# Performance work log

Hardware: AMD Instinct MI355X
Metric: run time of the kernel (lower is better)

Reference implementation:

```python
import jax, jax.numpy as jnp
import numpy as np

N = 50000
E = 1600000
EP = 500000
D_IN, D_EMB = 64, 32


def setup_inputs() -> dict:
    key = jax.random.key(0)
    ks = jax.random.split(key, 12)
    return {
        "x": jax.random.normal(ks[0], (N, D_IN), dtype=jnp.float32),
        "W1": jax.random.normal(ks[1], (D_IN, D_EMB), dtype=jnp.float32) * (1.0 / np.sqrt(D_IN)),
        "b1": jnp.zeros((D_EMB,), dtype=jnp.float32),
        "W2": jax.random.normal(ks[2], (D_EMB, 2 * D_EMB), dtype=jnp.float32) * (1.0 / np.sqrt(D_EMB)),
        "b2": jnp.zeros((2 * D_EMB,), dtype=jnp.float32),
        "eps": jax.random.normal(ks[3], (N, D_EMB), dtype=jnp.float32),
        "edge_src": jax.random.randint(ks[4], (E,), 0, N, dtype=jnp.int32),
        "edge_dst": jax.random.randint(ks[5], (E,), 0, N, dtype=jnp.int32),
        "pos_src": jax.random.randint(ks[6], (EP,), 0, N, dtype=jnp.int32),
        "pos_dst": jax.random.randint(ks[7], (EP,), 0, N, dtype=jnp.int32),
        "neg_src": jax.random.randint(ks[8], (EP,), 0, N, dtype=jnp.int32),
        "neg_dst": jax.random.randint(ks[9], (EP,), 0, N, dtype=jnp.int32),
    }


def _degree_norms(src, dst, n):
    ones = jnp.ones(src.shape, dtype=jnp.float32)
    out_deg = jax.ops.segment_sum(ones, src, num_segments=n)
    in_deg = jax.ops.segment_sum(ones, dst, num_segments=n)
    # DGL GraphConv norm='both': clamp degrees to >=1, pow(-0.5)
    return jnp.clip(out_deg, 1.0) ** -0.5, jnp.clip(in_deg, 1.0) ** -0.5


def _graph_conv(h, src, dst, norm_src, norm_dst, W, b, n):
    # rst = D_dst^{-1/2} A D_src^{-1/2} h W + b
    msg = (h * norm_src[:, None])[src]                       # [E, d] gather
    agg = jax.ops.segment_sum(msg, dst, num_segments=n)      # [N, d] scatter-add
    return (agg * norm_dst[:, None]) @ W + b


def _dot_predict(z, u, v):
    # u_dot_v: per-edge inner product of endpoint embeddings
    return jnp.sum(z[u] * z[v], axis=-1)


def reference(x, W1, b1, W2, b2, eps, edge_src, edge_dst,
              pos_src, pos_dst, neg_src, neg_dst):
    n = x.shape[0]
    ns, nd = _degree_norms(edge_src, edge_dst, n)
    h = _graph_conv(x, edge_src, edge_dst, ns, nd, W1, b1, n)
    h = jax.nn.relu(h)  # dropout = identity (eval mode)
    h = _graph_conv(h, edge_src, edge_dst, ns, nd, W2, b2, n)
    mu, log_var = jnp.split(h, 2, axis=-1)
    sigma = jnp.exp(log_var / 2.0)
    z = mu + sigma * eps
    pos = _dot_predict(z, pos_src, pos_dst)
    neg = _dot_predict(z, neg_src, neg_dst)
    return pos, neg, mu, sigma
```

## Files before the change

kernel.cpp:

```cpp
#include <hip/hip_runtime.h>
#include <math.h>

#define NN  50000
#define NE  1600000
#define NEP 500000
#define DIN 64
#define DE  32

#define BKT_SH 7
#define NB     391
#define S1B    250
#define CHK    6400
#define HB     128
#define HCHK   12500
#define HWRD   12500
#define XWB    3125

typedef float f4 __attribute__((ext_vector_type(4)));

__device__ __forceinline__ unsigned f2b(float f) {
    unsigned u = __float_as_uint(f);
    return (u + 0x7FFFu + ((u >> 16) & 1u)) >> 16;
}
__device__ __forceinline__ unsigned pack2(float a, float b) {
    return f2b(a) | (f2b(b) << 16);
}
__device__ __forceinline__ float blo(unsigned u) { return __uint_as_float(u << 16); }
__device__ __forceinline__ float bhi(unsigned u) { return __uint_as_float(u & 0xFFFF0000u); }

__global__ __launch_bounds__(256) void k_h1s1(const int* __restrict__ src,
                                              const int* __restrict__ dst,
                                              unsigned* __restrict__ partial,
                                              int* __restrict__ T) {
    __shared__ unsigned h[HWRD];
    int t = threadIdx.x;
    if (blockIdx.x < HB) {
        for (int i = t; i < HWRD; i += 256) h[i] = 0;
        __syncthreads();
        int beg = blockIdx.x * HCHK;
        const int ev = beg + HCHK;
        int i = beg + t;
        for (; i + 1792 < ev; i += 2048) {
            int s0 = src[i],        s1 = src[i + 256],  s2 = src[i + 512],  s3 = src[i + 768];
            int s4 = src[i + 1024], s5 = src[i + 1280], s6 = src[i + 1536], s7 = src[i + 1792];
            atomicAdd(&h[s0 >> 2], 1u << ((s0 & 3) * 8));
            atomicAdd(&h[s1 >> 2], 1u << ((s1 & 3) * 8));
            atomicAdd(&h[s2 >> 2], 1u << ((s2 & 3) * 8));
            atomicAdd(&h[s3 >> 2], 1u << ((s3 & 3) * 8));
            atomicAdd(&h[s4 >> 2], 1u << ((s4 & 3) * 8));
            atomicAdd(&h[s5 >> 2], 1u << ((s5 & 3) * 8));
            atomicAdd(&h[s6 >> 2], 1u << ((s6 & 3) * 8));
            atomicAdd(&h[s7 >> 2], 1u << ((s7 & 3) * 8));
        }
        for (; i < ev; i += 256) {
            int s = src[i];
            atomicAdd(&h[s >> 2], 1u << ((s & 3) * 8));
        }
        __syncthreads();
        unsigned* p = partial + (size_t)blockIdx.x * HWRD;
        for (int i2 = t; i2 < HWRD; i2 += 256) p[i2] = h[i2];
    } else {
        int b = blockIdx.x - HB;
        int* cd = (int*)h;
        for (int i = t; i < NB; i += 256) cd[i] = 0;
        __syncthreads();
        int beg = b * CHK;
        const int ev = beg + CHK;
        int i = beg + t;
        for (; i + 1792 < ev; i += 2048) {
            int d0 = dst[i],        d1 = dst[i + 256],  d2 = dst[i + 512],  d3 = dst[i + 768];
            int d4 = dst[i + 1024], d5 = dst[i + 1280], d6 = dst[i + 1536], d7 = dst[i + 1792];
            atomicAdd(&cd[d0 >> BKT_SH], 1);
            atomicAdd(&cd[d1 >> BKT_SH], 1);
            atomicAdd(&cd[d2 >> BKT_SH], 1);
            atomicAdd(&cd[d3 >> BKT_SH], 1);
            atomicAdd(&cd[d4 >> BKT_SH], 1);
            atomicAdd(&cd[d5 >> BKT_SH], 1);
            atomicAdd(&cd[d6 >> BKT_SH], 1);
            atomicAdd(&cd[d7 >> BKT_SH], 1);
        }
        for (; i < ev; i += 256)
            atomicAdd(&cd[dst[i] >> BKT_SH], 1);
        __syncthreads();
        for (int i2 = t; i2 < NB; i2 += 256) T[b * NB + i2] = cd[i2];
    }
}

__global__ __launch_bounds__(512) void k_s2h(const int* __restrict__ T,
                                             int* __restrict__ Base,
                                             int* __restrict__ BS,
                                             const unsigned* __restrict__ partial,
                                             int* __restrict__ degs) {
    int t = threadIdx.x;
    if (blockIdx.x == 0) {
        __shared__ int tot[512];
        int run = 0;
        if (t < NB) {
            for (int b = 0; b < S1B; b++) {
                Base[b * NB + t] = run;
                run += T[b * NB + t];
            }
        }
        tot[t] = (t < NB) ? run : 0;
        __syncthreads();
        for (int off = 1; off < 512; off <<= 1) {
            int v = (t >= off) ? tot[t - off] : 0;
            __syncthreads();
            tot[t] += v;
            __syncthreads();
        }
        if (t < NB) BS[t] = (t == 0) ? 0 : tot[t - 1];
        if (t == 0) BS[NB] = NE;
    } else {
        int w = (blockIdx.x - 1) * 512 + t;
        if (w < HWRD) {
            int c0 = 0, c1 = 0, c2 = 0, c3 = 0;
#pragma unroll 8
            for (int b = 0; b < HB; b++) {
                unsigned v = partial[(size_t)b * HWRD + w];
                c0 += (int)(v & 0xFFu);
                c1 += (int)((v >> 8) & 0xFFu);
                c2 += (int)((v >> 16) & 0xFFu);
                c3 += (int)(v >> 24);
            }
            ((int4*)degs)[w] = make_int4(c0, c1, c2, c3);
        }
    }
}

__global__ __launch_bounds__(512) void k_s3(const int* __restrict__ src,
                                            const int* __restrict__ dst,
                                            const int* __restrict__ T,
                                            const int* __restrict__ Base,
                                            const int* __restrict__ BS,
                                            unsigned* __restrict__ tmp) {
    __shared__ int scn[512];
    __shared__ int delta[NB];
    __shared__ int cur[NB];
    __shared__ unsigned buf[CHK];
    int t = threadIdx.x;
    int beg = blockIdx.x * CHK;
    scn[t] = (t < NB) ? T[blockIdx.x * NB + t] : 0;
    __syncthreads();
    for (int off = 1; off < 512; off <<= 1) {
        int v = (t >= off) ? scn[t - off] : 0;
        __syncthreads();
        scn[t] += v;
        __syncthreads();
    }
    if (t < NB) {
        int ls = (t == 0) ? 0 : scn[t - 1];
        cur[t] = ls;
        delta[t] = Base[blockIdx.x * NB + t] + BS[t] - ls;
    }
    __syncthreads();
    {
        const int ev = beg + CHK;
        int i = beg + t;
        for (; i + 1536 < ev; i += 2048) {
            int d0 = dst[i],        s0 = src[i];
            int d1 = dst[i + 512],  s1 = src[i + 512];
            int d2 = dst[i + 1024], s2 = src[i + 1024];
            int d3 = dst[i + 1536], s3 = src[i + 1536];
            int l0 = atomicAdd(&cur[d0 >> BKT_SH], 1); buf[l0] = (unsigned)s0 | ((unsigned)d0 << 16);
            int l1 = atomicAdd(&cur[d1 >> BKT_SH], 1); buf[l1] = (unsigned)s1 | ((unsigned)d1 << 16);
            int l2 = atomicAdd(&cur[d2 >> BKT_SH], 1); buf[l2] = (unsigned)s2 | ((unsigned)d2 << 16);
            int l3 = atomicAdd(&cur[d3 >> BKT_SH], 1); buf[l3] = (unsigned)s3 | ((unsigned)d3 << 16);
        }
        for (; i < ev; i += 512) {
            int d = dst[i];
            int s = src[i];
            int lp = atomicAdd(&cur[d >> BKT_SH], 1);
            buf[lp] = (unsigned)s | ((unsigned)d << 16);
        }
    }
    __syncthreads();
    for (int i = t; i < CHK; i += 512) {
        unsigned e = buf[i];
        tmp[delta[e >> (16 + BKT_SH)] + i] = e;
    }
}

__global__ __launch_bounds__(256) void k_s4x(const unsigned* __restrict__ tmp,
                                             const int* __restrict__ BS,
                                             int* __restrict__ csr,
                                             int* __restrict__ rowptr,
                                             const float* __restrict__ x,
                                             const float* __restrict__ W1,
                                             const int* __restrict__ degs,
                                             unsigned* __restrict__ xw1b) {
    __shared__ float sW[DIN * DE];
    int t = threadIdx.x;
    if (blockIdx.x < NB) {
        int* cnt = (int*)sW;
        int* scn = cnt + 128;
        int* cur = cnt + 256;
        int p = blockIdx.x;
        int ebeg = BS[p], eend = BS[p + 1];
        int ne = eend - ebeg;
        if (t < 128) cnt[t] = 0;
        __syncthreads();
        {
            int i = t;
            for (; i + 768 < ne; i += 1024) {
                unsigned e0 = tmp[ebeg + i];
                unsigned e1 = tmp[ebeg + i + 256];
                unsigned e2 = tmp[ebeg + i + 512];
                unsigned e3 = tmp[ebeg + i + 768];
                atomicAdd(&cnt[(e0 >> 16) & 127], 1);
                atomicAdd(&cnt[(e1 >> 16) & 127], 1);
                atomicAdd(&cnt[(e2 >> 16) & 127], 1);
                atomicAdd(&cnt[(e3 >> 16) & 127], 1);
            }
            for (; i < ne; i += 256)
                atomicAdd(&cnt[(tmp[ebeg + i] >> 16) & 127], 1);
        }
        __syncthreads();
        if (t < 128) scn[t] = cnt[t];
        __syncthreads();
        for (int off = 1; off < 128; off <<= 1) {
            int v = 0;
            if (t < 128 && t >= off) v = scn[t - off];
            __syncthreads();
            if (t < 128) scn[t] += v;
            __syncthreads();
        }
        if (t < 128) {
            int ex = (t == 0) ? 0 : scn[t - 1];
            cur[t] = ex;
            int node = (p << BKT_SH) + t;
            if (node < NN) rowptr[node] = ebeg + ex;
        }
        if (p == NB - 1 && t == 0) rowptr[NN] = NE;
        __syncthreads();
        {
            int i = t;
            for (; i + 768 < ne; i += 1024) {
                unsigned e0 = tmp[ebeg + i];
                unsigned e1 = tmp[ebeg + i + 256];
                unsigned e2 = tmp[ebeg + i + 512];
                unsigned e3 = tmp[ebeg + i + 768];
                int l0 = atomicAdd(&cur[(e0 >> 16) & 127], 1); csr[ebeg + l0] = (int)(e0 & 0xFFFFu);
                int l1 = atomicAdd(&cur[(e1 >> 16) & 127], 1); csr[ebeg + l1] = (int)(e1 & 0xFFFFu);
                int l2 = atomicAdd(&cur[(e2 >> 16) & 127], 1); csr[ebeg + l2] = (int)(e2 & 0xFFFFu);
                int l3 = atomicAdd(&cur[(e3 >> 16) & 127], 1); csr[ebeg + l3] = (int)(e3 & 0xFFFFu);
            }
            for (; i < ne; i += 256) {
                unsigned e = tmp[ebeg + i];
                int lp = atomicAdd(&cur[(e >> 16) & 127], 1);
                csr[ebeg + lp] = (int)(e & 0xFFFFu);
            }
        }
    } else {
        for (int i = t; i < DIN * DE; i += 256) sW[i] = W1[i];
        __syncthreads();
        int r  = (blockIdx.x - NB) * 16 + (t >> 4);
        int tc = t & 15;
        const float* xr = x + (size_t)r * DIN;
        float a0 = 0.f, a1 = 0.f;
#pragma unroll
        for (int k = 0; k < DIN; k++) {
            float v = xr[k];
            a0 += v * sW[k * DE + 2 * tc];
            a1 += v * sW[k * DE + 2 * tc + 1];
        }
        float ns = rsqrtf(fmaxf((float)degs[r], 1.0f));
        xw1b[r * 16 + tc] = pack2(a0 * ns, a1 * ns);
    }
}

__device__ __forceinline__ void acc8(float* a, uint4 w) {
    a[0] += blo(w.x); a[1] += bhi(w.x);
    a[2] += blo(w.y); a[3] += bhi(w.y);
    a[4] += blo(w.z); a[5] += bhi(w.z);
    a[6] += blo(w.w); a[7] += bhi(w.w);
}

__device__ __forceinline__ void gather_row(const int* __restrict__ csr,
                                           const uint4* __restrict__ msg,
                                           int beg, int end, int l, float* a) {
    int idx = beg;
    for (; idx + 8 <= end; idx += 8) {
        int s0 = csr[idx],     s1 = csr[idx + 1], s2 = csr[idx + 2], s3 = csr[idx + 3];
        int s4 = csr[idx + 4], s5 = csr[idx + 5], s6 = csr[idx + 6], s7 = csr[idx + 7];
        uint4 w0 = msg[s0 * 4 + l];
        uint4 w1 = msg[s1 * 4 + l];
        uint4 w2 = msg[s2 * 4 + l];
        uint4 w3 = msg[s3 * 4 + l];
        uint4 w4 = msg[s4 * 4 + l];
        uint4 w5 = msg[s5 * 4 + l];
        uint4 w6 = msg[s6 * 4 + l];
        uint4 w7 = msg[s7 * 4 + l];
        acc8(a, w0); acc8(a, w1); acc8(a, w2); acc8(a, w3);
        acc8(a, w4); acc8(a, w5); acc8(a, w6); acc8(a, w7);
    }
    for (; idx + 4 <= end; idx += 4) {
        int s0 = csr[idx], s1 = csr[idx + 1], s2 = csr[idx + 2], s3 = csr[idx + 3];
        uint4 w0 = msg[s0 * 4 + l];
        uint4 w1 = msg[s1 * 4 + l];
        uint4 w2 = msg[s2 * 4 + l];
        uint4 w3 = msg[s3 * 4 + l];
        acc8(a, w0); acc8(a, w1); acc8(a, w2); acc8(a, w3);
    }
    for (; idx < end; idx++) {
        uint4 w = msg[csr[idx] * 4 + l];
        acc8(a, w);
    }
}

__global__ __launch_bounds__(256) void k_g1(const int* __restrict__ rowptr,
                                            const int* __restrict__ csr,
                                            const uint4* __restrict__ msg,
                                            const int* __restrict__ degs,
                                            const float* __restrict__ b1,
                                            uint4* __restrict__ out) {
    int t = blockIdx.x * 256 + threadIdx.x;
    int r = t >> 3;
    int l = t & 3;
    int h = (t >> 2) & 1;
    if (r >= NN) return;
    int beg = rowptr[r];
    int end = rowptr[r + 1];
    int mid = beg + ((end - beg) >> 1);
    float a[8] = {0, 0, 0, 0, 0, 0, 0, 0};
    gather_row(csr, msg, h ? mid : beg, h ? end : mid, l, a);
#pragma unroll
    for (int k = 0; k < 8; k++) a[k] += __shfl_xor(a[k], 4);
    if (h) return;
    float scd = rsqrtf(fmaxf((float)(end - beg), 1.0f));
    float scs = rsqrtf(fmaxf((float)degs[r], 1.0f));
    const float4* b14 = (const float4*)b1;
    float4 bb0 = b14[2 * l], bb1 = b14[2 * l + 1];
    float o0 = fmaxf(scd * a[0] + bb0.x, 0.f) * scs;
    float o1 = fmaxf(scd * a[1] + bb0.y, 0.f) * scs;
    float o2 = fmaxf(scd * a[2] + bb0.z, 0.f) * scs;
    float o3 = fmaxf(scd * a[3] + bb0.w, 0.f) * scs;
    float o4 = fmaxf(scd * a[4] + bb1.x, 0.f) * scs;
    float o5 = fmaxf(scd * a[5] + bb1.y, 0.f) * scs;
    float o6 = fmaxf(scd * a[6] + bb1.z, 0.f) * scs;
    float o7 = fmaxf(scd * a[7] + bb1.w, 0.f) * scs;
    out[r * 4 + l] = make_uint4(pack2(o0, o1), pack2(o2, o3), pack2(o4, o5), pack2(o6, o7));
}

__global__ __launch_bounds__(256) void k_g2f(const int* __restrict__ rowptr,
                                             const int* __restrict__ csr,
                                             const uint4* __restrict__ msg,
                                             const float* __restrict__ W2,
                                             const float* __restrict__ b2,
                                             const float* __restrict__ eps,
                                             float* __restrict__ mu,
                                             float* __restrict__ sigma,
                                             unsigned* __restrict__ zb) {
    __shared__ float sW[DE * 64];
    __shared__ float sb[64];
    int t = threadIdx.x;
    for (int i = t; i < DE * 64; i += 256) sW[i] = W2[i];
    if (t < 64) sb[t] = b2[t];
    __syncthreads();
    int g = blockIdx.x * 256 + t;
    int r = g >> 3;
    int l = g & 3;
    int j = g & 7;
    int h = (g >> 2) & 1;
    if (r >= NN) return;
    int beg = rowptr[r];
    int end = rowptr[r + 1];
    int mid = beg + ((end - beg) >> 1);
    float a[8] = {0, 0, 0, 0, 0, 0, 0, 0};
    gather_row(csr, msg, h ? mid : beg, h ? end : mid, l, a);
#pragma unroll
    for (int k = 0; k < 8; k++) a[k] += __shfl_xor(a[k], 4);
    float scd = rsqrtf(fmaxf((float)(end - beg), 1.0f));
#pragma unroll
    for (int k = 0; k < 8; k++) a[k] *= scd;
    int cbase = 8 * j;
    float o3[8];
#pragma unroll
    for (int c = 0; c < 8; c++) o3[c] = sb[cbase + c];
#pragma unroll
    for (int d = 0; d < 4; d++) {
        int kb = 8 * (l ^ d);
#pragma unroll
        for (int k = 0; k < 8; k++) {
            float av = (d == 0) ? a[k] : __shfl_xor(a[k], d);
            const float* wrow = sW + (kb + k) * 64 + cbase;
#pragma unroll
            for (int c = 0; c < 8; c++) o3[c] += av * wrow[c];
        }
    }
    if (j < 4) {
        f4* mp = (f4*)(mu + (size_t)r * DE + cbase);
        f4 m0 = {o3[0], o3[1], o3[2], o3[3]};
        f4 m1 = {o3[4], o3[5], o3[6], o3[7]};
        __builtin_nontemporal_store(m0, mp);
        __builtin_nontemporal_store(m1, mp + 1);
    }
    float muv[8];
#pragma unroll
    for (int c = 0; c < 8; c++) muv[c] = __shfl_xor(o3[c], 4);
    if (j >= 4) {
        int cc = cbase - DE;
        const f4* ep = (const f4*)(eps + (size_t)r * DE + cc);
        f4 e0 = __builtin_nontemporal_load(ep);
        f4 e1 = __builtin_nontemporal_load(ep + 1);
        float ev[8] = {e0.x, e0.y, e0.z, e0.w, e1.x, e1.y, e1.z, e1.w};
        float sgv[8], zv[8];
#pragma unroll
        for (int c = 0; c < 8; c++) {
            sgv[c] = expf(0.5f * o3[c]);
            zv[c]  = muv[c] + sgv[c] * ev[c];
        }
        f4* sp = (f4*)(sigma + (size_t)r * DE + cc);
        f4 s0 = {sgv[0], sgv[1], sgv[2], sgv[3]};
        f4 s1 = {sgv[4], sgv[5], sgv[6], sgv[7]};
        __builtin_nontemporal_store(s0, sp);
        __builtin_nontemporal_store(s1, sp + 1);
        uint4* zp = (uint4*)(zb + (size_t)r * 16 + (j - 4) * 4);
        zp[0] = make_uint4(pack2(zv[0], zv[1]), pack2(zv[2], zv[3]),
                           pack2(zv[4], zv[5]), pack2(zv[6], zv[7]));
    }
}

__global__ __launch_bounds__(256) void k_dot2(const uint4* __restrict__ zb4,
                                              const int* __restrict__ pu,
                                              const int* __restrict__ pv,
                                              const int* __restrict__ nu,
                                              const int* __restrict__ nv,
                                              float* __restrict__ out) {
    int t = blockIdx.x * 256 + threadIdx.x;
    int e = t >> 2;
    int l = t & 3;
    if (e < 2 * NEP) {
        int ee = (e < NEP) ? e : e - NEP;
        const int* uu = (e < NEP) ? pu : nu;
        const int* vv = (e < NEP) ? pv : nv;
        int a = __builtin_nontemporal_load(uu + ee);
        int b = __builtin_nontemporal_load(vv + ee);
        uint4 za = zb4[a * 4 + l];
        uint4 zc = zb4[b * 4 + l];
        float s = blo(za.x) * blo(zc.x) + bhi(za.x) * bhi(zc.x)
                + blo(za.y) * blo(zc.y) + bhi(za.y) * bhi(zc.y)
                + blo(za.z) * blo(zc.z) + bhi(za.z) * bhi(zc.z)
                + blo(za.w) * blo(zc.w) + bhi(za.w) * bhi(zc.w);
        s += __shfl_xor(s, 1);
        s += __shfl_xor(s, 2);
        if (l == 0) __builtin_nontemporal_store(s, out + e);
    }
}

extern "C" void kernel_launch(void* const* d_in, const int* in_sizes, int n_in,
                              void* d_out, int out_size, void* d_ws, size_t ws_size,
                              hipStream_t stream) {
    const float* x    = (const float*)d_in[0];
    const float* W1   = (const float*)d_in[1];
    const float* b1   = (const float*)d_in[2];
    const float* W2   = (const float*)d_in[3];
    const float* b2   = (const float*)d_in[4];
    const float* eps  = (const float*)d_in[5];
    const int*   esrc = (const int*)d_in[6];
    const int*   edst = (const int*)d_in[7];
    const int*   psrc = (const int*)d_in[8];
    const int*   pdst = (const int*)d_in[9];
    const int*   gsrc = (const int*)d_in[10];
    const int*   gdst = (const int*)d_in[11];

    float* out = (float*)d_out;
    float* pos = out;
    float* mu  = out + 2 * NEP;
    float* sg  = out + 2 * NEP + NN * DE;

    int* wi = (int*)d_ws;
    int*      rowptr  = wi;
    int*      T       = wi + 50001;
    int*      Base    = wi + 147751;
    int*      BS      = wi + 245501;
    int*      degs    = wi + 245896;
    int*      csr     = wi + 295896;
    unsigned* partial = (unsigned*)(wi + 1895896);
    unsigned* tmp     = (unsigned*)(wi + 3495896);
    unsigned* P0      = (unsigned*)(wi + 5095896);
    unsigned* P1      = P0 + 16 * NN;

    k_h1s1<<<HB + S1B, 256, 0, stream>>>(esrc, edst, partial, T);
    k_s2h <<<1 + (HWRD + 511) / 512, 512, 0, stream>>>(T, Base, BS, partial, degs);
    k_s3  <<<S1B, 512, 0, stream>>>(esrc, edst, T, Base, BS, tmp);
    k_s4x <<<NB + XWB, 256, 0, stream>>>(tmp, BS, csr, rowptr, x, W1, degs, P0);
    k_g1  <<<(NN * 8 + 255) / 256, 256, 0, stream>>>(rowptr, csr, (const uint4*)P0, degs, b1, (uint4*)P1);
    k_g2f <<<(NN * 8 + 255) / 256, 256, 0, stream>>>(rowptr, csr, (const uint4*)P1, W2, b2, eps, mu, sg, P0);
    k_dot2<<<(2 * NEP * 4) / 256, 256, 0, stream>>>((const uint4*)P0, psrc, pdst, gsrc, gdst, pos);
}
```

Measured before the change: 204.6 us.

## Use 16-bit CSR indices and four-way split gather per row

Stores CSR source indices as ushort instead of int, which halves index traffic in both gather kernels. Each row is now handled by 16 lanes instead of 8: four groups take interleaved 8-edge chunks, and their partial sums are combined with an extra xor shuffle. In k_g2f each lane now computes 4 output columns instead of 8, and the scan in k_s2h is unrolled by five. The change adds more shuffles and doubles the thread count, and per-group work is coarse-grained for low-degree rows, with the tail handled by one group.

```diff
diff --git a/kernel.cpp b/kernel.cpp
--- a/kernel.cpp
+++ b/kernel.cpp
@@ -96,9 +96,17 @@
         __shared__ int tot[512];
         int run = 0;
         if (t < NB) {
-            for (int b = 0; b < S1B; b++) {
-                Base[b * NB + t] = run;
-                run += T[b * NB + t];
+            for (int b = 0; b < S1B; b += 5) {
+                int v0 = T[(b + 0) * NB + t];
+                int v1 = T[(b + 1) * NB + t];
+                int v2 = T[(b + 2) * NB + t];
+                int v3 = T[(b + 3) * NB + t];
+                int v4 = T[(b + 4) * NB + t];
+                Base[(b + 0) * NB + t] = run; run += v0;
+                Base[(b + 1) * NB + t] = run; run += v1;
+                Base[(b + 2) * NB + t] = run; run += v2;
+                Base[(b + 3) * NB + t] = run; run += v3;
+                Base[(b + 4) * NB + t] = run; run += v4;
             }
         }
         tot[t] = (t < NB) ? run : 0;
@@ -183,7 +191,7 @@
 
 __global__ __launch_bounds__(256) void k_s4x(const unsigned* __restrict__ tmp,
                                              const int* __restrict__ BS,
-                                             int* __restrict__ csr,
+                                             ushort* __restrict__ csr,
                                              int* __restrict__ rowptr,
                                              const float* __restrict__ x,
                                              const float* __restrict__ W1,
@@ -240,15 +248,15 @@
                 unsigned e1 = tmp[ebeg + i + 256];
                 unsigned e2 = tmp[ebeg + i + 512];
                 unsigned e3 = tmp[ebeg + i + 768];
-                int l0 = atomicAdd(&cur[(e0 >> 16) & 127], 1); csr[ebeg + l0] = (int)(e0 & 0xFFFFu);
-                int l1 = atomicAdd(&cur[(e1 >> 16) & 127], 1); csr[ebeg + l1] = (int)(e1 & 0xFFFFu);
-                int l2 = atomicAdd(&cur[(e2 >> 16) & 127], 1); csr[ebeg + l2] = (int)(e2 & 0xFFFFu);
-                int l3 = atomicAdd(&cur[(e3 >> 16) & 127], 1); csr[ebeg + l3] = (int)(e3 & 0xFFFFu);
+                int l0 = atomicAdd(&cur[(e0 >> 16) & 127], 1); csr[ebeg + l0] = (ushort)(e0 & 0xFFFFu);
+                int l1 = atomicAdd(&cur[(e1 >> 16) & 127], 1); csr[ebeg + l1] = (ushort)(e1 & 0xFFFFu);
+                int l2 = atomicAdd(&cur[(e2 >> 16) & 127], 1); csr[ebeg + l2] = (ushort)(e2 & 0xFFFFu);
+                int l3 = atomicAdd(&cur[(e3 >> 16) & 127], 1); csr[ebeg + l3] = (ushort)(e3 & 0xFFFFu);
             }
             for (; i < ne; i += 256) {
                 unsigned e = tmp[ebeg + i];
                 int lp = atomicAdd(&cur[(e >> 16) & 127], 1);
-                csr[ebeg + lp] = (int)(e & 0xFFFFu);
+                csr[ebeg + lp] = (ushort)(e & 0xFFFFu);
             }
         }
     } else {
@@ -276,13 +284,14 @@
     a[6] += blo(w.w); a[7] += bhi(w.w);
 }
 
-__device__ __forceinline__ void gather_row(const int* __restrict__ csr,
-                                           const uint4* __restrict__ msg,
-                                           int beg, int end, int l, float* a) {
-    int idx = beg;
-    for (; idx + 8 <= end; idx += 8) {
-        int s0 = csr[idx],     s1 = csr[idx + 1], s2 = csr[idx + 2], s3 = csr[idx + 3];
-        int s4 = csr[idx + 4], s5 = csr[idx + 5], s6 = csr[idx + 6], s7 = csr[idx + 7];
+__device__ __forceinline__ void gather_q(const ushort* __restrict__ crow,
+                                         const uint4* __restrict__ msg,
+                                         int len, int h, int l, float* a) {
+    int n8 = len >> 3;
+    for (int b = h; b < n8; b += 4) {
+        const ushort* p = crow + b * 8;
+        int s0 = p[0], s1 = p[1], s2 = p[2], s3 = p[3];
+        int s4 = p[4], s5 = p[5], s6 = p[6], s7 = p[7];
         uint4 w0 = msg[s0 * 4 + l];
         uint4 w1 = msg[s1 * 4 + l];
         uint4 w2 = msg[s2 * 4 + l];
@@ -294,40 +303,38 @@
         acc8(a, w0); acc8(a, w1); acc8(a, w2); acc8(a, w3);
         acc8(a, w4); acc8(a, w5); acc8(a, w6); acc8(a, w7);
     }
-    for (; idx + 4 <= end; idx += 4) {
-        int s0 = csr[idx], s1 = csr[idx + 1], s2 = csr[idx + 2], s3 = csr[idx + 3];
-        uint4 w0 = msg[s0 * 4 + l];
-        uint4 w1 = msg[s1 * 4 + l];
-        uint4 w2 = msg[s2 * 4 + l];
-        uint4 w3 = msg[s3 * 4 + l];
-        acc8(a, w0); acc8(a, w1); acc8(a, w2); acc8(a, w3);
-    }
-    for (; idx < end; idx++) {
-        uint4 w = msg[csr[idx] * 4 + l];
-        acc8(a, w);
+    int tail = len & 7;
+    if (tail && h == (n8 & 3)) {
+        const ushort* p = crow + n8 * 8;
+        for (int k = 0; k < tail; k++) {
+            uint4 w = msg[(int)p[k] * 4 + l];
+            acc8(a, w);
+        }
     }
 }
 
 __global__ __launch_bounds__(256) void k_g1(const int* __restrict__ rowptr,
-                                            const int* __restrict__ csr,
+                                            const ushort* __restrict__ csr,
                                             const uint4* __restrict__ msg,
                                             const int* __restrict__ degs,
                                             const float* __restrict__ b1,
                                             uint4* __restrict__ out) {
     int t = blockIdx.x * 256 + threadIdx.x;
-    int r = t >> 3;
+    int r = t >> 4;
     int l = t & 3;
-    int h = (t >> 2) & 1;
+    int h = (t >> 2) & 3;
     if (r >= NN) return;
     int beg = rowptr[r];
     int end = rowptr[r + 1];
-    int mid = beg + ((end - beg) >> 1);
+    int len = end - beg;
     float a[8] = {0, 0, 0, 0, 0, 0, 0, 0};
-    gather_row(csr, msg, h ? mid : beg, h ? end : mid, l, a);
+    gather_q(csr + beg, msg, len, h, l, a);
 #pragma unroll
     for (int k = 0; k < 8; k++) a[k] += __shfl_xor(a[k], 4);
+#pragma unroll
+    for (int k = 0; k < 8; k++) a[k] += __shfl_xor(a[k], 8);
     if (h) return;
-    float scd = rsqrtf(fmaxf((float)(end - beg), 1.0f));
+    float scd = rsqrtf(fmaxf((float)len, 1.0f));
     float scs = rsqrtf(fmaxf((float)degs[r], 1.0f));
     const float4* b14 = (const float4*)b1;
     float4 bb0 = b14[2 * l], bb1 = b14[2 * l + 1];
@@ -343,7 +350,7 @@
 }
 
 __global__ __launch_bounds__(256) void k_g2f(const int* __restrict__ rowptr,
-                                             const int* __restrict__ csr,
+                                             const ushort* __restrict__ csr,
                                              const uint4* __restrict__ msg,
                                              const float* __restrict__ W2,
                                              const float* __restrict__ b2,
@@ -358,25 +365,27 @@
     if (t < 64) sb[t] = b2[t];
     __syncthreads();
     int g = blockIdx.x * 256 + t;
-    int r = g >> 3;
+    int r = g >> 4;
     int l = g & 3;
-    int j = g & 7;
-    int h = (g >> 2) & 1;
+    int j = g & 15;
+    int h = (g >> 2) & 3;
     if (r >= NN) return;
     int beg = rowptr[r];
     int end = rowptr[r + 1];
-    int mid = beg + ((end - beg) >> 1);
+    int len = end - beg;
     float a[8] = {0, 0, 0, 0, 0, 0, 0, 0};
-    gather_row(csr, msg, h ? mid : beg, h ? end : mid, l, a);
+    gather_q(csr + beg, msg, len, h, l, a);
 #pragma unroll
     for (int k = 0; k < 8; k++) a[k] += __shfl_xor(a[k], 4);
-    float scd = rsqrtf(fmaxf((float)(end - beg), 1.0f));
+#pragma unroll
+    for (int k = 0; k < 8; k++) a[k] += __shfl_xor(a[k], 8);
+    float scd = rsqrtf(fmaxf((float)len, 1.0f));
 #pragma unroll
     for (int k = 0; k < 8; k++) a[k] *= scd;
-    int cbase = 8 * j;
-    float o3[8];
-#pragma unroll
-    for (int c = 0; c < 8; c++) o3[c] = sb[cbase + c];
+    int cbase = 4 * j;
+    float o3[4];
+#pragma unroll
+    for (int c = 0; c < 4; c++) o3[c] = sb[cbase + c];
 #pragma unroll
     for (int d = 0; d < 4; d++) {
         int kb = 8 * (l ^ d);
@@ -385,39 +394,33 @@
             float av = (d == 0) ? a[k] : __shfl_xor(a[k], d);
             const float* wrow = sW + (kb + k) * 64 + cbase;
 #pragma unroll
-            for (int c = 0; c < 8; c++) o3[c] += av * wrow[c];
-        }
-    }
-    if (j < 4) {
+            for (int c = 0; c < 4; c++) o3[c] += av * wrow[c];
+        }
+    }
+    if (j < 8) {
         f4* mp = (f4*)(mu + (size_t)r * DE + cbase);
         f4 m0 = {o3[0], o3[1], o3[2], o3[3]};
-        f4 m1 = {o3[4], o3[5], o3[6], o3[7]};
         __builtin_nontemporal_store(m0, mp);
-        __builtin_nontemporal_store(m1, mp + 1);
-    }
-    float muv[8];
-#pragma unroll
-    for (int c = 0; c < 8; c++) muv[c] = __shfl_xor(o3[c], 4);
-    if (j >= 4) {
+    }
+    float muv[4];
+#pragma unroll
+    for (int c = 0; c < 4; c++) muv[c] = __shfl_xor(o3[c], 8);
+    if (j >= 8) {
         int cc = cbase - DE;
         const f4* ep = (const f4*)(eps + (size_t)r * DE + cc);
         f4 e0 = __builtin_nontemporal_load(ep);
-        f4 e1 = __builtin_nontemporal_load(ep + 1);
-        float ev[8] = {e0.x, e0.y, e0.z, e0.w, e1.x, e1.y, e1.z, e1.w};
-        float sgv[8], zv[8];
-#pragma unroll
-        for (int c = 0; c < 8; c++) {
+        float ev[4] = {e0.x, e0.y, e0.z, e0.w};
+        float sgv[4], zv[4];
+#pragma unroll
+        for (int c = 0; c < 4; c++) {
             sgv[c] = expf(0.5f * o3[c]);
             zv[c]  = muv[c] + sgv[c] * ev[c];
         }
         f4* sp = (f4*)(sigma + (size_t)r * DE + cc);
         f4 s0 = {sgv[0], sgv[1], sgv[2], sgv[3]};
-        f4 s1 = {sgv[4], sgv[5], sgv[6], sgv[7]};
         __builtin_nontemporal_store(s0, sp);
-        __builtin_nontemporal_store(s1, sp + 1);
-        uint4* zp = (uint4*)(zb + (size_t)r * 16 + (j - 4) * 4);
-        zp[0] = make_uint4(pack2(zv[0], zv[1]), pack2(zv[2], zv[3]),
-                           pack2(zv[4], zv[5]), pack2(zv[6], zv[7]));
+        uint2* zp = (uint2*)(zb + (size_t)r * 16 + (j - 8) * 2);
+        *zp = make_uint2(pack2(zv[0], zv[1]), pack2(zv[2], zv[3]));
     }
 }
 
@@ -475,7 +478,7 @@
     int*      Base    = wi + 147751;
     int*      BS      = wi + 245501;
     int*      degs    = wi + 245896;
-    int*      csr     = wi + 295896;
+    ushort*   csr     = (ushort*)(wi + 295896);
     unsigned* partial = (unsigned*)(wi + 1895896);
     unsigned* tmp     = (unsigned*)(wi + 3495896);
     unsigned* P0      = (unsigned*)(wi + 5095896);
@@ -485,7 +488,7 @@
     k_s2h <<<1 + (HWRD + 511) / 512, 512, 0, stream>>>(T, Base, BS, partial, degs);
     k_s3  <<<S1B, 512, 0, stream>>>(esrc, edst, T, Base, BS, tmp);
     k_s4x <<<NB + XWB, 256, 0, stream>>>(tmp, BS, csr, rowptr, x, W1, degs, P0);
-    k_g1  <<<(NN * 8 + 255) / 256, 256, 0, stream>>>(rowptr, csr, (const uint4*)P0, degs, b1, (uint4*)P1);
-    k_g2f <<<(NN * 8 + 255) / 256, 256, 0, stream>>>(rowptr, csr, (const uint4*)P1, W2, b2, eps, mu, sg, P0);
+    k_g1  <<<(NN * 16 + 255) / 256, 256, 0, stream>>>(rowptr, csr, (const uint4*)P0, degs, b1, (uint4*)P1);
+    k_g2f <<<(NN * 16 + 255) / 256, 256, 0, stream>>>(rowptr, csr, (const uint4*)P1, W2, b2, eps, mu, sg, P0);
     k_dot2<<<(2 * NEP * 4) / 256, 256, 0, stream>>>((const uint4*)P0, psrc, pdst, gsrc, gdst, pos);
 }
```

Measured after the change: 211.0 us. 3.1% more time.

## Use padded 16-bit CSR rows with in-degree histogram and vectorized index loads

Applied to the files above, without the earlier changes.

The in-degree is now computed with the same packed byte histogram used for out-degree. A small scan block in k_s3 builds row offsets padded to multiples of 8. This removes the per-bucket counting and scan pass from k_s4x, which now scatters 16-bit source indices straight into the padded CSR. The gather kernels read eight indices per 16-byte load and split them between the two half-threads, which halves index bandwidth at the cost of an extra dst histogram pass, padding space, and buffer aliasing between partialD and tmp.

```diff
diff --git a/kernel.cpp b/kernel.cpp
--- a/kernel.cpp
+++ b/kernel.cpp
@@ -30,19 +30,24 @@
 
 __global__ __launch_bounds__(256) void k_h1s1(const int* __restrict__ src,
                                               const int* __restrict__ dst,
-                                              unsigned* __restrict__ partial,
+                                              unsigned* __restrict__ partialS,
+                                              unsigned* __restrict__ partialD,
                                               int* __restrict__ T) {
     __shared__ unsigned h[HWRD];
     int t = threadIdx.x;
-    if (blockIdx.x < HB) {
+    if (blockIdx.x < 2 * HB) {
+        int isS = blockIdx.x < HB;
+        int chunk = isS ? blockIdx.x : blockIdx.x - HB;
+        const int* e = isS ? src : dst;
+        unsigned* pout = (isS ? partialS : partialD) + (size_t)chunk * HWRD;
         for (int i = t; i < HWRD; i += 256) h[i] = 0;
         __syncthreads();
-        int beg = blockIdx.x * HCHK;
+        int beg = chunk * HCHK;
         const int ev = beg + HCHK;
         int i = beg + t;
         for (; i + 1792 < ev; i += 2048) {
-            int s0 = src[i],        s1 = src[i + 256],  s2 = src[i + 512],  s3 = src[i + 768];
-            int s4 = src[i + 1024], s5 = src[i + 1280], s6 = src[i + 1536], s7 = src[i + 1792];
+            int s0 = e[i],        s1 = e[i + 256],  s2 = e[i + 512],  s3 = e[i + 768];
+            int s4 = e[i + 1024], s5 = e[i + 1280], s6 = e[i + 1536], s7 = e[i + 1792];
             atomicAdd(&h[s0 >> 2], 1u << ((s0 & 3) * 8));
             atomicAdd(&h[s1 >> 2], 1u << ((s1 & 3) * 8));
             atomicAdd(&h[s2 >> 2], 1u << ((s2 & 3) * 8));
@@ -53,14 +58,13 @@
             atomicAdd(&h[s7 >> 2], 1u << ((s7 & 3) * 8));
         }
         for (; i < ev; i += 256) {
-            int s = src[i];
+            int s = e[i];
             atomicAdd(&h[s >> 2], 1u << ((s & 3) * 8));
         }
         __syncthreads();
-        unsigned* p = partial + (size_t)blockIdx.x * HWRD;
-        for (int i2 = t; i2 < HWRD; i2 += 256) p[i2] = h[i2];
+        for (int i2 = t; i2 < HWRD; i2 += 256) pout[i2] = h[i2];
     } else {
-        int b = blockIdx.x - HB;
+        int b = blockIdx.x - 2 * HB;
         int* cd = (int*)h;
         for (int i = t; i < NB; i += 256) cd[i] = 0;
         __syncthreads();
@@ -89,16 +93,26 @@
 __global__ __launch_bounds__(512) void k_s2h(const int* __restrict__ T,
                                              int* __restrict__ Base,
                                              int* __restrict__ BS,
-                                             const unsigned* __restrict__ partial,
-                                             int* __restrict__ degs) {
+                                             const unsigned* __restrict__ partialS,
+                                             const unsigned* __restrict__ partialD,
+                                             int* __restrict__ dout,
+                                             int* __restrict__ din) {
     int t = threadIdx.x;
     if (blockIdx.x == 0) {
         __shared__ int tot[512];
         int run = 0;
         if (t < NB) {
-            for (int b = 0; b < S1B; b++) {
-                Base[b * NB + t] = run;
-                run += T[b * NB + t];
+            for (int b = 0; b < S1B; b += 5) {
+                int v0 = T[(b + 0) * NB + t];
+                int v1 = T[(b + 1) * NB + t];
+                int v2 = T[(b + 2) * NB + t];
+                int v3 = T[(b + 3) * NB + t];
+                int v4 = T[(b + 4) * NB + t];
+                Base[(b + 0) * NB + t] = run; run += v0;
+                Base[(b + 1) * NB + t] = run; run += v1;
+                Base[(b + 2) * NB + t] = run; run += v2;
+                Base[(b + 3) * NB + t] = run; run += v3;
+                Base[(b + 4) * NB + t] = run; run += v4;
             }
         }
         tot[t] = (t < NB) ? run : 0;
@@ -112,18 +126,21 @@
         if (t < NB) BS[t] = (t == 0) ? 0 : tot[t - 1];
         if (t == 0) BS[NB] = NE;
     } else {
-        int w = (blockIdx.x - 1) * 512 + t;
+        int half = blockIdx.x >= 26;
+        int w = ((half ? blockIdx.x - 26 : blockIdx.x - 1)) * 512 + t;
+        const unsigned* p = half ? partialD : partialS;
+        int* dd = half ? din : dout;
         if (w < HWRD) {
             int c0 = 0, c1 = 0, c2 = 0, c3 = 0;
 #pragma unroll 8
             for (int b = 0; b < HB; b++) {
-                unsigned v = partial[(size_t)b * HWRD + w];
+                unsigned v = p[(size_t)b * HWRD + w];
                 c0 += (int)(v & 0xFFu);
                 c1 += (int)((v >> 8) & 0xFFu);
                 c2 += (int)((v >> 16) & 0xFFu);
                 c3 += (int)(v >> 24);
             }
-            ((int4*)degs)[w] = make_int4(c0, c1, c2, c3);
+            ((int4*)dd)[w] = make_int4(c0, c1, c2, c3);
         }
     }
 }
@@ -133,123 +150,114 @@
                                             const int* __restrict__ T,
                                             const int* __restrict__ Base,
                                             const int* __restrict__ BS,
-                                            unsigned* __restrict__ tmp) {
+                                            unsigned* __restrict__ tmp,
+                                            const int* __restrict__ din,
+                                            int* __restrict__ prow) {
     __shared__ int scn[512];
     __shared__ int delta[NB];
     __shared__ int cur[NB];
     __shared__ unsigned buf[CHK];
     int t = threadIdx.x;
-    int beg = blockIdx.x * CHK;
-    scn[t] = (t < NB) ? T[blockIdx.x * NB + t] : 0;
-    __syncthreads();
-    for (int off = 1; off < 512; off <<= 1) {
-        int v = (t >= off) ? scn[t - off] : 0;
-        __syncthreads();
-        scn[t] += v;
-        __syncthreads();
-    }
-    if (t < NB) {
-        int ls = (t == 0) ? 0 : scn[t - 1];
-        cur[t] = ls;
-        delta[t] = Base[blockIdx.x * NB + t] + BS[t] - ls;
-    }
-    __syncthreads();
-    {
-        const int ev = beg + CHK;
-        int i = beg + t;
-        for (; i + 1536 < ev; i += 2048) {
-            int d0 = dst[i],        s0 = src[i];
-            int d1 = dst[i + 512],  s1 = src[i + 512];
-            int d2 = dst[i + 1024], s2 = src[i + 1024];
-            int d3 = dst[i + 1536], s3 = src[i + 1536];
-            int l0 = atomicAdd(&cur[d0 >> BKT_SH], 1); buf[l0] = (unsigned)s0 | ((unsigned)d0 << 16);
-            int l1 = atomicAdd(&cur[d1 >> BKT_SH], 1); buf[l1] = (unsigned)s1 | ((unsigned)d1 << 16);
-            int l2 = atomicAdd(&cur[d2 >> BKT_SH], 1); buf[l2] = (unsigned)s2 | ((unsigned)d2 << 16);
-            int l3 = atomicAdd(&cur[d3 >> BKT_SH], 1); buf[l3] = (unsigned)s3 | ((unsigned)d3 << 16);
-        }
-        for (; i < ev; i += 512) {
-            int d = dst[i];
-            int s = src[i];
-            int lp = atomicAdd(&cur[d >> BKT_SH], 1);
-            buf[lp] = (unsigned)s | ((unsigned)d << 16);
-        }
-    }
-    __syncthreads();
-    for (int i = t; i < CHK; i += 512) {
-        unsigned e = buf[i];
-        tmp[delta[e >> (16 + BKT_SH)] + i] = e;
+    if (blockIdx.x < S1B) {
+        int beg = blockIdx.x * CHK;
+        scn[t] = (t < NB) ? T[blockIdx.x * NB + t] : 0;
+        __syncthreads();
+        for (int off = 1; off < 512; off <<= 1) {
+            int v = (t >= off) ? scn[t - off] : 0;
+            __syncthreads();
+            scn[t] += v;
+            __syncthreads();
+        }
+        if (t < NB) {
+            int ls = (t == 0) ? 0 : scn[t - 1];
+            cur[t] = ls;
+            delta[t] = Base[blockIdx.x * NB + t] + BS[t] - ls;
+        }
+        __syncthreads();
+        {
+            const int ev = beg + CHK;
+            int i = beg + t;
+            for (; i + 1536 < ev; i += 2048) {
+                int d0 = dst[i],        s0 = src[i];
+                int d1 = dst[i + 512],  s1 = src[i + 512];
+                int d2 = dst[i + 1024], s2 = src[i + 1024];
+                int d3 = dst[i + 1536], s3 = src[i + 1536];
+                int l0 = atomicAdd(&cur[d0 >> BKT_SH], 1); buf[l0] = (unsigned)s0 | ((unsigned)d0 << 16);
+                int l1 = atomicAdd(&cur[d1 >> BKT_SH], 1); buf[l1] = (unsigned)s1 | ((unsigned)d1 << 16);
+                int l2 = atomicAdd(&cur[d2 >> BKT_SH], 1); buf[l2] = (unsigned)s2 | ((unsigned)d2 << 16);
+                int l3 = atomicAdd(&cur[d3 >> BKT_SH], 1); buf[l3] = (unsigned)s3 | ((unsigned)d3 << 16);
+            }
+            for (; i < ev; i += 512) {
+                int d = dst[i];
+                int s = src[i];
+                int lp = atomicAdd(&cur[d >> BKT_SH], 1);
+                buf[lp] = (unsigned)s | ((unsigned)d << 16);
+            }
+        }
+        __syncthreads();
+        for (int i = t; i < CHK; i += 512) {
+            unsigned e = buf[i];
+            tmp[delta[e >> (16 + BKT_SH)] + i] = e;
+        }
+    } else {
+        int base = t * 98;
+        int n = NN - base;
+        if (n > 98) n = 98;
+        if (n < 0) n = 0;
+        int loc = 0;
+        for (int i = 0; i < n; i++) loc += (din[base + i] + 7) & ~7;
+        scn[t] = loc;
+        __syncthreads();
+        for (int off = 1; off < 512; off <<= 1) {
+            int v = (t >= off) ? scn[t - off] : 0;
+            __syncthreads();
+            scn[t] += v;
+            __syncthreads();
+        }
+        int run = scn[t] - loc;
+        for (int i = 0; i < n; i++) {
+            int d8 = (din[base + i] + 7) & ~7;
+            prow[base + i] = run;
+            run += d8;
+        }
     }
 }
 
 __global__ __launch_bounds__(256) void k_s4x(const unsigned* __restrict__ tmp,
                                              const int* __restrict__ BS,
-                                             int* __restrict__ csr,
-                                             int* __restrict__ rowptr,
+                                             const int* __restrict__ prow,
+                                             ushort* __restrict__ csr,
                                              const float* __restrict__ x,
                                              const float* __restrict__ W1,
-                                             const int* __restrict__ degs,
+                                             const int* __restrict__ dout,
                                              unsigned* __restrict__ xw1b) {
     __shared__ float sW[DIN * DE];
     int t = threadIdx.x;
     if (blockIdx.x < NB) {
-        int* cnt = (int*)sW;
-        int* scn = cnt + 128;
-        int* cur = cnt + 256;
+        int* cur = (int*)sW;
         int p = blockIdx.x;
+        if (t < 128) {
+            int node = (p << BKT_SH) + t;
+            cur[t] = (node < NN) ? prow[node] : 0;
+        }
+        __syncthreads();
         int ebeg = BS[p], eend = BS[p + 1];
         int ne = eend - ebeg;
-        if (t < 128) cnt[t] = 0;
-        __syncthreads();
-        {
-            int i = t;
-            for (; i + 768 < ne; i += 1024) {
-                unsigned e0 = tmp[ebeg + i];
-                unsigned e1 = tmp[ebeg + i + 256];
-                unsigned e2 = tmp[ebeg + i + 512];
-                unsigned e3 = tmp[ebeg + i + 768];
-                atomicAdd(&cnt[(e0 >> 16) & 127], 1);
-                atomicAdd(&cnt[(e1 >> 16) & 127], 1);
-                atomicAdd(&cnt[(e2 >> 16) & 127], 1);
-                atomicAdd(&cnt[(e3 >> 16) & 127], 1);
-            }
-            for (; i < ne; i += 256)
-                atomicAdd(&cnt[(tmp[ebeg + i] >> 16) & 127], 1);
-        }
-        __syncthreads();
-        if (t < 128) scn[t] = cnt[t];
-        __syncthreads();
-        for (int off = 1; off < 128; off <<= 1) {
-            int v = 0;
-            if (t < 128 && t >= off) v = scn[t - off];
-            __syncthreads();
-            if (t < 128) scn[t] += v;
-            __syncthreads();
-        }
-        if (t < 128) {
-            int ex = (t == 0) ? 0 : scn[t - 1];
-            cur[t] = ex;
-            int node = (p << BKT_SH) + t;
-            if (node < NN) rowptr[node] = ebeg + ex;
-        }
-        if (p == NB - 1 && t == 0) rowptr[NN] = NE;
-        __syncthreads();
-        {
-            int i = t;
-            for (; i + 768 < ne; i += 1024) {
-                unsigned e0 = tmp[ebeg + i];
-                unsigned e1 = tmp[ebeg + i + 256];
-                unsigned e2 = tmp[ebeg + i + 512];
-                unsigned e3 = tmp[ebeg + i + 768];
-                int l0 = atomicAdd(&cur[(e0 >> 16) & 127], 1); csr[ebeg + l0] = (int)(e0 & 0xFFFFu);
-                int l1 = atomicAdd(&cur[(e1 >> 16) & 127], 1); csr[ebeg + l1] = (int)(e1 & 0xFFFFu);
-                int l2 = atomicAdd(&cur[(e2 >> 16) & 127], 1); csr[ebeg + l2] = (int)(e2 & 0xFFFFu);
-                int l3 = atomicAdd(&cur[(e3 >> 16) & 127], 1); csr[ebeg + l3] = (int)(e3 & 0xFFFFu);
-            }
-            for (; i < ne; i += 256) {
-                unsigned e = tmp[ebeg + i];
-                int lp = atomicAdd(&cur[(e >> 16) & 127], 1);
-                csr[ebeg + lp] = (int)(e & 0xFFFFu);
-            }
+        int i = t;
+        for (; i + 768 < ne; i += 1024) {
+            unsigned e0 = tmp[ebeg + i];
+            unsigned e1 = tmp[ebeg + i + 256];
+            unsigned e2 = tmp[ebeg + i + 512];
+            unsigned e3 = tmp[ebeg + i + 768];
+            int l0 = atomicAdd(&cur[(e0 >> 16) & 127], 1); csr[l0] = (ushort)(e0 & 0xFFFFu);
+            int l1 = atomicAdd(&cur[(e1 >> 16) & 127], 1); csr[l1] = (ushort)(e1 & 0xFFFFu);
+            int l2 = atomicAdd(&cur[(e2 >> 16) & 127], 1); csr[l2] = (ushort)(e2 & 0xFFFFu);
+            int l3 = atomicAdd(&cur[(e3 >> 16) & 127], 1); csr[l3] = (ushort)(e3 & 0xFFFFu);
+        }
+        for (; i < ne; i += 256) {
+            unsigned e = tmp[ebeg + i];
+            int lp = atomicAdd(&cur[(e >> 16) & 127], 1);
+            csr[lp] = (ushort)(e & 0xFFFFu);
         }
     } else {
         for (int i = t; i < DIN * DE; i += 256) sW[i] = W1[i];
@@ -264,7 +272,7 @@
             a0 += v * sW[k * DE + 2 * tc];
             a1 += v * sW[k * DE + 2 * tc + 1];
         }
-        float ns = rsqrtf(fmaxf((float)degs[r], 1.0f));
+        float ns = rsqrtf(fmaxf((float)dout[r], 1.0f));
         xw1b[r * 16 + tc] = pack2(a0 * ns, a1 * ns);
     }
 }
@@ -276,13 +284,17 @@
     a[6] += blo(w.w); a[7] += bhi(w.w);
 }
 
-__device__ __forceinline__ void gather_row(const int* __restrict__ csr,
-                                           const uint4* __restrict__ msg,
-                                           int beg, int end, int l, float* a) {
-    int idx = beg;
-    for (; idx + 8 <= end; idx += 8) {
-        int s0 = csr[idx],     s1 = csr[idx + 1], s2 = csr[idx + 2], s3 = csr[idx + 3];
-        int s4 = csr[idx + 4], s5 = csr[idx + 5], s6 = csr[idx + 6], s7 = csr[idx + 7];
+__device__ __forceinline__ void gather_half(const ushort* __restrict__ crow,
+                                            const uint4* __restrict__ msg,
+                                            int len, int h, int l, float* a) {
+    int nb = len >> 3;
+    const uint4* cp = (const uint4*)crow;
+    for (int b = h; b < nb; b += 2) {
+        uint4 cw = cp[b];
+        int s0 = (int)(cw.x & 0xFFFFu), s1 = (int)(cw.x >> 16);
+        int s2 = (int)(cw.y & 0xFFFFu), s3 = (int)(cw.y >> 16);
+        int s4 = (int)(cw.z & 0xFFFFu), s5 = (int)(cw.z >> 16);
+        int s6 = (int)(cw.w & 0xFFFFu), s7 = (int)(cw.w >> 16);
         uint4 w0 = msg[s0 * 4 + l];
         uint4 w1 = msg[s1 * 4 + l];
         uint4 w2 = msg[s2 * 4 + l];
@@ -294,24 +306,21 @@
         acc8(a, w0); acc8(a, w1); acc8(a, w2); acc8(a, w3);
         acc8(a, w4); acc8(a, w5); acc8(a, w6); acc8(a, w7);
     }
-    for (; idx + 4 <= end; idx += 4) {
-        int s0 = csr[idx], s1 = csr[idx + 1], s2 = csr[idx + 2], s3 = csr[idx + 3];
-        uint4 w0 = msg[s0 * 4 + l];
-        uint4 w1 = msg[s1 * 4 + l];
-        uint4 w2 = msg[s2 * 4 + l];
-        uint4 w3 = msg[s3 * 4 + l];
-        acc8(a, w0); acc8(a, w1); acc8(a, w2); acc8(a, w3);
-    }
-    for (; idx < end; idx++) {
-        uint4 w = msg[csr[idx] * 4 + l];
-        acc8(a, w);
-    }
-}
-
-__global__ __launch_bounds__(256) void k_g1(const int* __restrict__ rowptr,
-                                            const int* __restrict__ csr,
+    int tail = len & 7;
+    if (tail && h == (nb & 1)) {
+        const ushort* tp = crow + nb * 8;
+        for (int k = 0; k < tail; k++) {
+            uint4 w = msg[(int)tp[k] * 4 + l];
+            acc8(a, w);
+        }
+    }
+}
+
+__global__ __launch_bounds__(256) void k_g1(const int* __restrict__ prow,
+                                            const int* __restrict__ din,
+                                            const int* __restrict__ dout,
+                                            const ushort* __restrict__ csr,
                                             const uint4* __restrict__ msg,
-                                            const int* __restrict__ degs,
                                             const float* __restrict__ b1,
                                             uint4* __restrict__ out) {
     int t = blockIdx.x * 256 + threadIdx.x;
@@ -319,16 +328,14 @@
     int l = t & 3;
     int h = (t >> 2) & 1;
     if (r >= NN) return;
-    int beg = rowptr[r];
-    int end = rowptr[r + 1];
-    int mid = beg + ((end - beg) >> 1);
+    int len = din[r];
     float a[8] = {0, 0, 0, 0, 0, 0, 0, 0};
-    gather_row(csr, msg, h ? mid : beg, h ? end : mid, l, a);
+    gather_half(csr + prow[r], msg, len, h, l, a);
 #pragma unroll
     for (int k = 0; k < 8; k++) a[k] += __shfl_xor(a[k], 4);
     if (h) return;
-    float scd = rsqrtf(fmaxf((float)(end - beg), 1.0f));
-    float scs = rsqrtf(fmaxf((float)degs[r], 1.0f));
+    float scd = rsqrtf(fmaxf((float)len, 1.0f));
+    float scs = rsqrtf(fmaxf((float)dout[r], 1.0f));
     const float4* b14 = (const float4*)b1;
     float4 bb0 = b14[2 * l], bb1 = b14[2 * l + 1];
     float o0 = fmaxf(scd * a[0] + bb0.x, 0.f) * scs;
@@ -342,8 +349,9 @@
     out[r * 4 + l] = make_uint4(pack2(o0, o1), pack2(o2, o3), pack2(o4, o5), pack2(o6, o7));
 }
 
-__global__ __launch_bounds__(256) void k_g2f(const int* __restrict__ rowptr,
-                                             const int* __restrict__ csr,
+__global__ __launch_bounds__(256) void k_g2f(const int* __restrict__ prow,
+                                             const int* __restrict__ din,
+                                             const ushort* __restrict__ csr,
                                              const uint4* __restrict__ msg,
                                              const float* __restrict__ W2,
                                              const float* __restrict__ b2,
@@ -363,14 +371,12 @@
     int j = g & 7;
     int h = (g >> 2) & 1;
     if (r >= NN) return;
-    int beg = rowptr[r];
-    int end = rowptr[r + 1];
-    int mid = beg + ((end - beg) >> 1);
+    int len = din[r];
     float a[8] = {0, 0, 0, 0, 0, 0, 0, 0};
-    gather_row(csr, msg, h ? mid : beg, h ? end : mid, l, a);
+    gather_half(csr + prow[r], msg, len, h, l, a);
 #pragma unroll
     for (int k = 0; k < 8; k++) a[k] += __shfl_xor(a[k], 4);
-    float scd = rsqrtf(fmaxf((float)(end - beg), 1.0f));
+    float scd = rsqrtf(fmaxf((float)len, 1.0f));
 #pragma unroll
     for (int k = 0; k < 8; k++) a[k] *= scd;
     int cbase = 8 * j;
@@ -470,22 +476,24 @@
     float* sg  = out + 2 * NEP + NN * DE;
 
     int* wi = (int*)d_ws;
-    int*      rowptr  = wi;
-    int*      T       = wi + 50001;
-    int*      Base    = wi + 147751;
-    int*      BS      = wi + 245501;
-    int*      degs    = wi + 245896;
-    int*      csr     = wi + 295896;
-    unsigned* partial = (unsigned*)(wi + 1895896);
-    unsigned* tmp     = (unsigned*)(wi + 3495896);
-    unsigned* P0      = (unsigned*)(wi + 5095896);
-    unsigned* P1      = P0 + 16 * NN;
-
-    k_h1s1<<<HB + S1B, 256, 0, stream>>>(esrc, edst, partial, T);
-    k_s2h <<<1 + (HWRD + 511) / 512, 512, 0, stream>>>(T, Base, BS, partial, degs);
-    k_s3  <<<S1B, 512, 0, stream>>>(esrc, edst, T, Base, BS, tmp);
-    k_s4x <<<NB + XWB, 256, 0, stream>>>(tmp, BS, csr, rowptr, x, W1, degs, P0);
-    k_g1  <<<(NN * 8 + 255) / 256, 256, 0, stream>>>(rowptr, csr, (const uint4*)P0, degs, b1, (uint4*)P1);
-    k_g2f <<<(NN * 8 + 255) / 256, 256, 0, stream>>>(rowptr, csr, (const uint4*)P1, W2, b2, eps, mu, sg, P0);
+    int*      dout_    = wi;
+    int*      din      = wi + 50000;
+    int*      prow     = wi + 100000;
+    int*      T        = wi + 150000;
+    int*      Base     = wi + 247750;
+    int*      BS       = wi + 345500;
+    ushort*   csr      = (ushort*)(wi + 345896);
+    unsigned* partialS = (unsigned*)(wi + 1320896);
+    unsigned* partialD = (unsigned*)(wi + 2920896);
+    unsigned* tmp      = (unsigned*)(wi + 2920896);
+    unsigned* P0       = (unsigned*)(wi + 4520896);
+    unsigned* P1       = P0 + 16 * NN;
+
+    k_h1s1<<<2 * HB + S1B, 256, 0, stream>>>(esrc, edst, partialS, partialD, T);
+    k_s2h <<<51, 512, 0, stream>>>(T, Base, BS, partialS, partialD, dout_, din);
+    k_s3  <<<S1B + 1, 512, 0, stream>>>(esrc, edst, T, Base, BS, tmp, din, prow);
+    k_s4x <<<NB + XWB, 256, 0, stream>>>(tmp, BS, prow, csr, x, W1, dout_, P0);
+    k_g1  <<<(NN * 8 + 255) / 256, 256, 0, stream>>>(prow, din, dout_, csr, (const uint4*)P0, b1, (uint4*)P1);
+    k_g2f <<<(NN * 8 + 255) / 256, 256, 0, stream>>>(prow, din, csr, (const uint4*)P1, W2, b2, eps, mu, sg, P0);
     k_dot2<<<(2 * NEP * 4) / 256, 256, 0, stream>>>((const uint4*)P0, psrc, pdst, gsrc, gdst, pos);
 }
```

Measured after the change: 269.9 us. 1.32x slower.
